# Optimization experiments

Hardware: AMD Instinct MI355X
Metric: run time of the kernel (lower is better)

The kernel has to match this reference:

```python
import jax, jax.numpy as jnp
import numpy as np

N = 50000   # nodes
E = 800000  # edges
G = 64      # graphs in batch
H = 64      # hidden_dim
IN = 4      # input_dim (degree-derived features)


def setup_inputs() -> dict:
    key = jax.random.key(0)
    ks = jax.random.split(key, 9)
    src = jax.random.randint(ks[0], (E,), 0, N, dtype=jnp.int32)
    dst = jax.random.randint(ks[1], (E,), 0, N, dtype=jnp.int32)
    graph_ids = jnp.sort(jax.random.randint(ks[2], (N,), 0, G, dtype=jnp.int32))

    def glorot(k, shape):
        fan_in = shape[0]
        return jax.random.normal(k, shape, jnp.float32) / np.float32(np.sqrt(fan_in))

    return dict(
        src=src, dst=dst, graph_ids=graph_ids,
        W1=glorot(ks[3], (IN, H)), b1=jnp.zeros((H,), jnp.float32),
        W2=glorot(ks[4], (H, H)),  b2=jnp.zeros((H,), jnp.float32),
        W3=glorot(ks[5], (H, H)),  b3=jnp.zeros((H,), jnp.float32),
        W4=glorot(ks[6], (H, H)),  b4=jnp.zeros((H,), jnp.float32),
        Wout=glorot(ks[7], (H, 1)), bout=jnp.zeros((1,), jnp.float32),
    )


def _graph_conv(h, src, dst, norm_src, norm_dst, W, b):
    # DGL GraphConv, norm='both': D_dst^{-1/2} * A^T * (D_src^{-1/2} * h) @ W + b
    m = (h * norm_src)[src]                              # [E, F] gather
    agg = jax.ops.segment_sum(m, dst, num_segments=N)    # [N, F] scatter-add
    return (agg * norm_dst) @ W + b


def reference(src, dst, graph_ids, W1, b1, W2, b2, W3, b3, W4, b4, Wout, bout):
    ones_e = jnp.ones((E,), jnp.float32)
    in_deg = jax.ops.segment_sum(ones_e, dst, num_segments=N)   # [N]
    out_deg = jax.ops.segment_sum(ones_e, src, num_segments=N)  # [N]

    # degree-derived node features (exactly as in forward)
    h1 = in_deg[:, None]
    h2 = (in_deg - 3.0 > 0).astype(jnp.float32)[:, None]
    h3 = 3.0 / h1
    h4 = (in_deg - 4.0 > 0).astype(jnp.float32)[:, None]
    h_ = jnp.concatenate([h1, h2, h3, h4], axis=1)               # [N, 4]

    # symmetric norms (DGL clamps degree to >= 1)
    norm_src = jnp.clip(out_deg, 1.0, None)[:, None] ** -0.5     # [N, 1]
    norm_dst = jnp.clip(in_deg, 1.0, None)[:, None] ** -0.5      # [N, 1]

    h = jax.nn.relu(_graph_conv(h_, src, dst, norm_src, norm_dst, W1, b1))
    h = jax.nn.relu(_graph_conv(h, src, dst, norm_src, norm_dst, W2, b2))
    h = jax.nn.relu(_graph_conv(h, src, dst, norm_src, norm_dst, W3, b3))
    h = jax.nn.relu(_graph_conv(h, src, dst, norm_src, norm_dst, W4, b4))

    # dgl.mean_nodes: per-graph mean pooling
    node_counts = jax.ops.segment_sum(jnp.ones((N,), jnp.float32), graph_ids, num_segments=G)
    graph_emb = jax.ops.segment_sum(h, graph_ids, num_segments=G) / node_counts[:, None]

    # dropout = identity at inference
    return jax.nn.sigmoid(graph_emb @ Wout + bout)               # [G, 1]
```

## Files before the change

kernel.cpp:

```cpp
#include <hip/hip_runtime.h>
#include <hip/hip_fp8.h>
#include <math.h>

#define N_NODES 50000
#define N_EDGES 800000
#define NP 4
#define NS 64
#define PSZ (N_NODES / NP)
#define SSZ (N_EDGES / NS)
#define NB 196

typedef _Float16 half8 __attribute__((ext_vector_type(8)));
typedef float floatx4 __attribute__((ext_vector_type(4)));

__device__ __forceinline__ unsigned char f_to_fp8(float f) {
    __hip_fp8_e4m3 q(f);
    return (unsigned char)q.__x;
}
__device__ __forceinline__ float fp8_to_f(unsigned char u) {
    __hip_fp8_e4m3 q;
    q.__x = (__hip_fp8_storage_t)u;
    return (float)q;
}

__global__ __launch_bounds__(256) void hist_wt_kernel(const int* __restrict__ src,
                                                      const int* __restrict__ dst,
                                                      unsigned char* __restrict__ inpart,
                                                      unsigned char* __restrict__ outpart,
                                                      unsigned char* __restrict__ rank,
                                                      const float* __restrict__ W2,
                                                      const float* __restrict__ W3,
                                                      const float* __restrict__ W4,
                                                      _Float16* __restrict__ WT,
                                                      float* __restrict__ gacc) {
    __shared__ int h[PSZ + 4];
    if (blockIdx.x >= NP * NS) {
        int wb = blockIdx.x - NP * NS;
        if (wb < 48) {
            int i = wb * 256 + threadIdx.x;
            if (i < 3 * 4096) {
                int l = i >> 12;
                int r = i & 4095;
                int k = r >> 6, n = r & 63;
                const float* W = (l == 0) ? W2 : (l == 1) ? W3 : W4;
                WT[l * 4096 + n * 64 + k] = (_Float16)W[r];
            }
        } else {
            for (int i = threadIdx.x; i < 64 * 64 + 64; i += 256) gacc[i] = 0.0f;
        }
        return;
    }
    int p = blockIdx.x / NS, s = blockIdx.x % NS;
    for (int i = threadIdx.x; i < (PSZ + 4) / 4; i += 256)
        ((int4*)h)[i] = make_int4(0, 0, 0, 0);
    __syncthreads();
    int lo = p * PSZ;
    int ebase = s * SSZ;
    const int4* d4 = (const int4*)(dst + ebase);
    const int4* s4 = (const int4*)(src + ebase);
    unsigned char* rk = rank + ebase;
    for (int i = threadIdx.x; i < SSZ / 4; i += 256) {
        int4 d = d4[i];
        int4 sv = s4[i];
        int t;
        t = d.x - lo;  if ((unsigned)t < PSZ) rk[4 * i + 0] = (unsigned char)(atomicAdd(&h[t], 1) & 0xffff);
        t = d.y - lo;  if ((unsigned)t < PSZ) rk[4 * i + 1] = (unsigned char)(atomicAdd(&h[t], 1) & 0xffff);
        t = d.z - lo;  if ((unsigned)t < PSZ) rk[4 * i + 2] = (unsigned char)(atomicAdd(&h[t], 1) & 0xffff);
        t = d.w - lo;  if ((unsigned)t < PSZ) rk[4 * i + 3] = (unsigned char)(atomicAdd(&h[t], 1) & 0xffff);
        t = sv.x - lo; if ((unsigned)t < PSZ) atomicAdd(&h[t], 0x10000);
        t = sv.y - lo; if ((unsigned)t < PSZ) atomicAdd(&h[t], 0x10000);
        t = sv.z - lo; if ((unsigned)t < PSZ) atomicAdd(&h[t], 0x10000);
        t = sv.w - lo; if ((unsigned)t < PSZ) atomicAdd(&h[t], 0x10000);
    }
    __syncthreads();
    unsigned char* ip = inpart + (size_t)s * N_NODES + lo;
    unsigned char* op = outpart + (size_t)s * N_NODES + lo;
    for (int i = threadIdx.x; i < PSZ / 2; i += 256) {
        int v0 = h[2 * i], v1 = h[2 * i + 1];
        uchar2 iv, ov;
        iv.x = (unsigned char)(v0 & 0xff);
        iv.y = (unsigned char)(v1 & 0xff);
        ov.x = (unsigned char)((v0 >> 16) & 0xff);
        ov.y = (unsigned char)((v1 >> 16) & 0xff);
        ((uchar2*)ip)[i] = iv;
        ((uchar2*)op)[i] = ov;
    }
}

__global__ void scan_block_feat_kernel(unsigned char* __restrict__ inpart,
                                       const unsigned char* __restrict__ outpart,
                                       const int* __restrict__ graph_ids,
                                       int* __restrict__ row_start, int* __restrict__ blk_sums,
                                       float* __restrict__ norm_src, float* __restrict__ norm_dst,
                                       uchar4* __restrict__ hs0, float* __restrict__ gcnt, int N) {
    __shared__ int ghist[64];
    if (threadIdx.x < 64) ghist[threadIdx.x] = 0;
    int i = blockIdx.x * 256 + threadIdx.x;
    int din_i = 0, dout_i = 0;
    if (i < N) {
        unsigned char run = 0;
#pragma unroll
        for (int s = 0; s < NS; ++s) {
            unsigned char c = inpart[(size_t)s * N_NODES + i];
            inpart[(size_t)s * N_NODES + i] = run;
            run = (unsigned char)(run + c);
            dout_i += outpart[(size_t)s * N_NODES + i];
        }
        din_i = (int)run;
        float din = (float)din_i;
        float dout = (float)dout_i;
        float ns = 1.0f / sqrtf(fmaxf(dout, 1.0f));
        float nd = 1.0f / sqrtf(fmaxf(din, 1.0f));
        norm_src[i] = ns;
        norm_dst[i] = nd;
        float h1 = din;
        float h2 = (din - 3.0f > 0.0f) ? 1.0f : 0.0f;
        float h3 = 3.0f / din;
        float h4 = (din - 4.0f > 0.0f) ? 1.0f : 0.0f;
        uchar4 q;
        q.x = f_to_fp8(h1 * ns);
        q.y = f_to_fp8(h2 * ns);
        q.z = f_to_fp8(h3 * ns);
        q.w = f_to_fp8(h4 * ns);
        hs0[i] = q;
    }
    __syncthreads();
    if (i < N) atomicAdd(&ghist[graph_ids[i]], 1);
    int lane = threadIdx.x & 63;
    int wid = threadIdx.x >> 6;
    int x = din_i;
#pragma unroll
    for (int off = 1; off < 64; off <<= 1) {
        int t = __shfl_up(x, off);
        if (lane >= off) x += t;
    }
    __shared__ int wsum[4];
    if (lane == 63) wsum[wid] = x;
    __syncthreads();
    int woff = 0;
    for (int w = 0; w < wid; ++w) woff += wsum[w];
    int incl = x + woff;
    if (i < N) row_start[i] = incl - din_i;
    if (threadIdx.x == 255) blk_sums[blockIdx.x] = incl;
    if (threadIdx.x < 64 && ghist[threadIdx.x] > 0)
        atomicAdd(&gcnt[threadIdx.x], (float)ghist[threadIdx.x]);
}

__global__ void row_add_kernel(int* __restrict__ row_start,
                               const int* __restrict__ blk_sums, int N) {
    __shared__ int sOff[256];
    int t = threadIdx.x;
    int v = (t < NB) ? blk_sums[t] : 0;
    int lane = t & 63;
    int wid = t >> 6;
    int x = v;
#pragma unroll
    for (int off = 1; off < 64; off <<= 1) {
        int tt = __shfl_up(x, off);
        if (lane >= off) x += tt;
    }
    __shared__ int wsum[4];
    if (lane == 63) wsum[wid] = x;
    __syncthreads();
    int woff = 0;
    for (int w = 0; w < wid; ++w) woff += wsum[w];
    sOff[t] = x + woff - v;
    __syncthreads();
    int i = blockIdx.x * 256 + threadIdx.x;
    if (blockIdx.x == 0 && threadIdx.x == 0) row_start[N] = N_EDGES;
    if (i < N) row_start[i] += sOff[blockIdx.x];
}

__global__ __launch_bounds__(256) void csr_fill_kernel(const int* __restrict__ src,
                                                       const int* __restrict__ dst,
                                                       const int* __restrict__ row_start,
                                                       const unsigned char* __restrict__ inpart,
                                                       const unsigned char* __restrict__ rank,
                                                       unsigned short* __restrict__ csr_src) {
    int i = blockIdx.x * 256 + threadIdx.x;
    if (i >= N_EDGES / 4) return;
    int4 d = ((const int4*)dst)[i];
    int4 sv = ((const int4*)src)[i];
    uchar4 rk = ((const uchar4*)rank)[i];
    int s = (4 * i) / SSZ;
    const unsigned char* pref = inpart + (size_t)s * N_NODES;
    csr_src[row_start[d.x] + (int)pref[d.x] + (int)rk.x] = (unsigned short)sv.x;
    csr_src[row_start[d.y] + (int)pref[d.y] + (int)rk.y] = (unsigned short)sv.y;
    csr_src[row_start[d.z] + (int)pref[d.z] + (int)rk.z] = (unsigned short)sv.z;
    csr_src[row_start[d.w] + (int)pref[d.w] + (int)rk.w] = (unsigned short)sv.w;
}

__global__ __launch_bounds__(256) void conv4_kernel(const unsigned char* __restrict__ hs0,
                                                    const int* __restrict__ row_start,
                                                    const unsigned short* __restrict__ csr_src,
                                                    const float* __restrict__ norm_src,
                                                    const float* __restrict__ norm_dst,
                                                    const float* __restrict__ W,
                                                    const float* __restrict__ b,
                                                    unsigned char* __restrict__ out, int N) {
    __shared__ float sW[4 * 64];
    __shared__ float sb[64];
    sW[threadIdx.x] = W[threadIdx.x];
    if (threadIdx.x < 64) sb[threadIdx.x] = b[threadIdx.x];

    const int lane = threadIdx.x & 63;
    const int wavei = threadIdx.x >> 6;
    const int l16 = lane & 15;
    const int node = blockIdx.x * 16 + wavei * 4 + (lane >> 4);

    const int rs = row_start[node];
    const int deg = row_start[node + 1] - rs;
    const int ncg = (deg + 15) >> 4;

    float a0 = 0.f, a1 = 0.f, a2 = 0.f, a3 = 0.f;
    for (int c = 0; c < ncg; ++c) {
        int off = c * 16 + l16;
        unsigned pos = (unsigned)(rs + off);
        if (pos > (unsigned)(N_EDGES - 1)) pos = N_EDGES - 1;
        unsigned idx = csr_src[pos];
        unsigned tv = *(const unsigned*)(hs0 + ((size_t)idx << 2));
        if (off >= deg) tv = 0u;
        a0 += fp8_to_f((unsigned char)(tv & 0xff));
        a1 += fp8_to_f((unsigned char)((tv >> 8) & 0xff));
        a2 += fp8_to_f((unsigned char)((tv >> 16) & 0xff));
        a3 += fp8_to_f((unsigned char)((tv >> 24) & 0xff));
    }
#pragma unroll
    for (int o = 1; o < 16; o <<= 1) {
        a0 += __shfl_xor(a0, o);
        a1 += __shfl_xor(a1, o);
        a2 += __shfl_xor(a2, o);
        a3 += __shfl_xor(a3, o);
    }
    __syncthreads();
    float nd = norm_dst[node];
    float ns = norm_src[node];
    uchar4 q;
    unsigned char* qp = (unsigned char*)&q;
#pragma unroll
    for (int j = 0; j < 4; ++j) {
        int f = l16 * 4 + j;
        float r = sb[f] + nd * (a0 * sW[f] + a1 * sW[64 + f] +
                                a2 * sW[128 + f] + a3 * sW[192 + f]);
        qp[j] = f_to_fp8(fmaxf(r, 0.0f) * ns);
    }
    *(uchar4*)(out + (size_t)node * 64 + l16 * 4) = q;
}

__global__ __launch_bounds__(256) void conv64_kernel(
        const unsigned char* __restrict__ hs_in,
        const int* __restrict__ row_start,
        const unsigned short* __restrict__ csr_src,
        const float* __restrict__ norm_src,
        const float* __restrict__ norm_dst,
        const _Float16* __restrict__ WT, const float* __restrict__ b,
        unsigned char* __restrict__ out8,
        const int* __restrict__ graph_ids, float* __restrict__ gacc,
        int do_pool, int N) {
    __shared__ _Float16 sAgg[16][72];
    const int lane = threadIdx.x & 63;
    const int wavei = __builtin_amdgcn_readfirstlane(threadIdx.x >> 6);
    const int l16 = lane & 15;
    const int gsel = (lane >> 4);
    const int vblock = blockIdx.x * 16;
    const int node = vblock + wavei * 4 + gsel;

    const int rs = row_start[node];
    const int deg = row_start[node + 1] - rs;

    int ncg = (deg + 15) >> 4;
    int m1 = max(ncg, __shfl_xor(ncg, 16));
    int ncw = max(m1, __shfl_xor(m1, 32));

    float acc0 = 0.f, acc1 = 0.f, acc2 = 0.f, acc3 = 0.f;
    const int blane = (lane & 48);

    int pos = rs + l16;
    unsigned pc = (unsigned)pos;
    if (pc > (unsigned)(N_EDGES - 1)) pc = N_EDGES - 1;
    int idx = (int)csr_src[pc];

    for (int c = 0; c < ncw; ++c) {
        int posN = rs + (c + 1) * 16 + l16;
        unsigned pn = (unsigned)posN;
        if (pn > (unsigned)(N_EDGES - 1)) pn = N_EDGES - 1;
        int idxN = (int)csr_src[pn];

        unsigned tv0, tv1, tv2, tv3, tv4, tv5, tv6, tv7;
        unsigned tv8, tv9, tv10, tv11, tv12, tv13, tv14, tv15;
#define GLOAD(J, TV)                                                        \
        {                                                                   \
            int si = __shfl(idx, blane + (J));                              \
            TV = *(const unsigned*)(hs_in + (((size_t)(unsigned)si) << 6)   \
                                    + (l16 << 2));                          \
        }
        GLOAD(0, tv0)   GLOAD(1, tv1)   GLOAD(2, tv2)   GLOAD(3, tv3)
        GLOAD(4, tv4)   GLOAD(5, tv5)   GLOAD(6, tv6)   GLOAD(7, tv7)
        GLOAD(8, tv8)   GLOAD(9, tv9)   GLOAD(10, tv10) GLOAD(11, tv11)
        GLOAD(12, tv12) GLOAD(13, tv13) GLOAD(14, tv14) GLOAD(15, tv15)
#undef GLOAD
        int cbase = c * 16;
#define ACC(J, TV)                                                          \
        {                                                                   \
            float mk = (cbase + (J) < deg) ? 1.0f : 0.0f;                   \
            acc0 += mk * fp8_to_f((unsigned char)(TV & 0xff));              \
            acc1 += mk * fp8_to_f((unsigned char)((TV >> 8) & 0xff));       \
            acc2 += mk * fp8_to_f((unsigned char)((TV >> 16) & 0xff));      \
            acc3 += mk * fp8_to_f((unsigned char)((TV >> 24) & 0xff));      \
        }
        ACC(0, tv0)   ACC(1, tv1)   ACC(2, tv2)   ACC(3, tv3)
        ACC(4, tv4)   ACC(5, tv5)   ACC(6, tv6)   ACC(7, tv7)
        ACC(8, tv8)   ACC(9, tv9)   ACC(10, tv10) ACC(11, tv11)
        ACC(12, tv12) ACC(13, tv13) ACC(14, tv14) ACC(15, tv15)
#undef ACC
        idx = idxN;
    }

    float nd = norm_dst[node];
    _Float16 f0 = (_Float16)(acc0 * nd);
    _Float16 f1 = (_Float16)(acc1 * nd);
    _Float16 f2 = (_Float16)(acc2 * nd);
    _Float16 f3 = (_Float16)(acc3 * nd);
    _Float16* rowp = &sAgg[wavei * 4 + gsel][l16 * 4];
    rowp[0] = f0; rowp[1] = f1; rowp[2] = f2; rowp[3] = f3;
    __syncthreads();

    const int l15 = lane & 15;
    const int quad = lane >> 4;
    const _Float16* aRow = &sAgg[l15][quad * 8];
    half8 a0 = *(const half8*)(aRow);
    half8 a1 = *(const half8*)(aRow + 32);

    const _Float16* bp = WT + ((size_t)(wavei * 16 + l15)) * 64 + quad * 8;
    half8 b0 = *(const half8*)bp;
    half8 b1 = *(const half8*)(bp + 32);

    floatx4 cc = (floatx4){0.f, 0.f, 0.f, 0.f};
    cc = __builtin_amdgcn_mfma_f32_16x16x32_f16(a0, b0, cc, 0, 0, 0);
    cc = __builtin_amdgcn_mfma_f32_16x16x32_f16(a1, b1, cc, 0, 0, 0);

    const int col = wavei * 16 + l15;
    float bias = b[col];

    if (do_pool) {
        int g0 = graph_ids[vblock];
        int g15 = graph_ids[vblock + 15];
        if (g0 == g15) {
            float fsum = 0.0f;
#pragma unroll
            for (int r = 0; r < 4; ++r)
                fsum += fmaxf(cc[r] + bias, 0.0f);
            fsum += __shfl_xor(fsum, 16);
            fsum += __shfl_xor(fsum, 32);
            if (quad == 0)
                atomicAdd(&gacc[g0 * 64 + col], fsum);
        } else {
#pragma unroll
            for (int r = 0; r < 4; ++r) {
                int m = quad * 4 + r;
                float val = fmaxf(cc[r] + bias, 0.0f);
                atomicAdd(&gacc[graph_ids[vblock + m] * 64 + col], val);
            }
        }
    } else {
#pragma unroll
        for (int r = 0; r < 4; ++r) {
            int m = quad * 4 + r;
            int v = vblock + m;
            float val = fmaxf(cc[r] + bias, 0.0f) * norm_src[v];
            out8[(size_t)v * 64 + col] = f_to_fp8(val);
        }
    }
}

__global__ void pool2_kernel(const float* __restrict__ gacc, const float* __restrict__ gcnt,
                             const float* __restrict__ Wout, const float* __restrict__ bout,
                             float* __restrict__ out) {
    int lane = threadIdx.x & 63;
    int g = blockIdx.x * 4 + (threadIdx.x >> 6);
    float p = (gacc[g * 64 + lane] / gcnt[g]) * Wout[lane];
#pragma unroll
    for (int off = 32; off; off >>= 1) p += __shfl_xor(p, off);
    if (lane == 0) out[g] = 1.0f / (1.0f + expf(-(p + bout[0])));
}

extern "C" void kernel_launch(void* const* d_in, const int* in_sizes, int n_in,
                              void* d_out, int out_size, void* d_ws, size_t ws_size,
                              hipStream_t stream) {
    const int* src = (const int*)d_in[0];
    const int* dst = (const int*)d_in[1];
    const int* graph_ids = (const int*)d_in[2];
    const float* W1 = (const float*)d_in[3];
    const float* b1 = (const float*)d_in[4];
    const float* W2 = (const float*)d_in[5];
    const float* b2 = (const float*)d_in[6];
    const float* W3 = (const float*)d_in[7];
    const float* b3 = (const float*)d_in[8];
    const float* W4 = (const float*)d_in[9];
    const float* b4 = (const float*)d_in[10];
    const float* Wout = (const float*)d_in[11];
    const float* bout = (const float*)d_in[12];
    float* out = (float*)d_out;

    const int N = N_NODES, E = N_EDGES;

    unsigned char* buf8A = (unsigned char*)d_ws;
    unsigned char* buf8B = buf8A + (size_t)N * 64;
    _Float16* WT   = (_Float16*)(buf8B + (size_t)N * 64);
    float* gacc = (float*)(WT + 3 * 4096);
    float* gcnt = gacc + 64 * 64;
    unsigned char* hs0 = (unsigned char*)(gcnt + 64);
    float* norm_src = (float*)(hs0 + (size_t)N * 4);
    float* norm_dst = norm_src + N;
    unsigned short* csr_src = (unsigned short*)(norm_dst + N);
    int* row_start = (int*)(csr_src + E);
    int* blk_sums  = row_start + (N + 1);
    unsigned char* inpart  = (unsigned char*)(blk_sums + NB + 1);
    unsigned char* outpart = inpart + (size_t)NS * N;
    unsigned char* rank    = outpart + (size_t)NS * N;

    hist_wt_kernel<<<NP * NS + 49, 256, 0, stream>>>(src, dst, inpart, outpart, rank,
                                                     W2, W3, W4, WT, gacc);
    scan_block_feat_kernel<<<NB, 256, 0, stream>>>(inpart, outpart, graph_ids,
                                                   row_start, blk_sums,
                                                   norm_src, norm_dst, (uchar4*)hs0, gcnt, N);
    row_add_kernel<<<NB, 256, 0, stream>>>(row_start, blk_sums, N);
    csr_fill_kernel<<<(E / 4 + 255) / 256, 256, 0, stream>>>(src, dst, row_start, inpart,
                                                             rank, csr_src);

    const int CB = N / 16;
    conv4_kernel<<<CB, 256, 0, stream>>>(hs0, row_start, csr_src,
                                         norm_src, norm_dst, W1, b1, buf8A, N);
    conv64_kernel<<<CB, 256, 0, stream>>>(buf8A, row_start, csr_src, norm_src, norm_dst,
                                          WT + 0 * 4096, b2, buf8B, graph_ids, gacc, 0, N);
    conv64_kernel<<<CB, 256, 0, stream>>>(buf8B, row_start, csr_src, norm_src, norm_dst,
                                          WT + 1 * 4096, b3, buf8A, graph_ids, gacc, 0, N);
    conv64_kernel<<<CB, 256, 0, stream>>>(buf8A, row_start, csr_src, norm_src, norm_dst,
                                          WT + 2 * 4096, b4, (unsigned char*)nullptr,
                                          graph_ids, gacc, 1, N);

    pool2_kernel<<<16, 256, 0, stream>>>(gacc, gcnt, Wout, bout, out);
}
```

Measured before the change: 184.3 us.

## Restructure conv64 gather to 8 lanes per node with double-buffered 8-byte loads

The 64-feature aggregation kernel now assigns 8 lanes per destination node, each loading 8 fp8 features as a uint2, so a wave covers 8 nodes instead of 4. Gathers are double-buffered: the next chunk of neighbor rows is loaded while the previous one is accumulated. Blocks shrink to 2 waves of 128 threads, and each wave does two MFMA column tiles in the dense transform. The aim is more memory-level parallelism and fewer idle lanes on low-degree nodes, at the cost of more registers per thread and more padding waste when degrees within a wave differ.

New measurement: 184.9 us. About the same (+0.4%).

```diff
diff --git a/kernel.cpp b/kernel.cpp
--- a/kernel.cpp
+++ b/kernel.cpp
@@ -247,7 +247,37 @@
     *(uchar4*)(out + (size_t)node * 64 + l16 * 4) = q;
 }
 
-__global__ __launch_bounds__(256) void conv64_kernel(
+#define GLOAD8(T, IDX)                                                     \
+    _Pragma("unroll")                                                      \
+    for (int j = 0; j < 8; ++j) {                                          \
+        int si = __shfl(IDX, blane + j);                                   \
+        T[j] = *(const uint2*)(hs_in + (((size_t)(unsigned)si) << 6)       \
+                               + (l8 << 3));                               \
+    }
+
+#define ACCUM8(T, CB)                                                      \
+    _Pragma("unroll")                                                      \
+    for (int j = 0; j < 8; ++j) {                                          \
+        float mk = ((CB) + j < deg) ? 1.0f : 0.0f;                         \
+        unsigned lo_ = T[j].x, hi_ = T[j].y;                               \
+        acc0 += mk * fp8_to_f((unsigned char)(lo_ & 0xff));                \
+        acc1 += mk * fp8_to_f((unsigned char)((lo_ >> 8) & 0xff));         \
+        acc2 += mk * fp8_to_f((unsigned char)((lo_ >> 16) & 0xff));        \
+        acc3 += mk * fp8_to_f((unsigned char)((lo_ >> 24) & 0xff));        \
+        acc4 += mk * fp8_to_f((unsigned char)(hi_ & 0xff));                \
+        acc5 += mk * fp8_to_f((unsigned char)((hi_ >> 8) & 0xff));         \
+        acc6 += mk * fp8_to_f((unsigned char)((hi_ >> 16) & 0xff));        \
+        acc7 += mk * fp8_to_f((unsigned char)((hi_ >> 24) & 0xff));        \
+    }
+
+#define LOADI8(DST, C)                                                     \
+    {                                                                      \
+        unsigned p_ = (unsigned)(rs + (C) * 8 + l8);                       \
+        if (p_ > (unsigned)(N_EDGES - 1)) p_ = N_EDGES - 1;                \
+        DST = (int)csr_src[p_];                                            \
+    }
+
+__global__ __launch_bounds__(128) void conv64_kernel(
         const unsigned char* __restrict__ hs_in,
         const int* __restrict__ row_start,
         const unsigned short* __restrict__ csr_src,
@@ -260,69 +290,51 @@
     __shared__ _Float16 sAgg[16][72];
     const int lane = threadIdx.x & 63;
     const int wavei = __builtin_amdgcn_readfirstlane(threadIdx.x >> 6);
-    const int l16 = lane & 15;
-    const int gsel = (lane >> 4);
+    const int l8 = lane & 7;
+    const int gsel = lane >> 3;
+    const int blane = lane & 56;
     const int vblock = blockIdx.x * 16;
-    const int node = vblock + wavei * 4 + gsel;
+    const int node = vblock + wavei * 8 + gsel;
 
     const int rs = row_start[node];
     const int deg = row_start[node + 1] - rs;
 
-    int ncg = (deg + 15) >> 4;
-    int m1 = max(ncg, __shfl_xor(ncg, 16));
+    int ncg = (deg + 7) >> 3;
+    int m1 = max(ncg, __shfl_xor(ncg, 8));
+    m1 = max(m1, __shfl_xor(m1, 16));
     int ncw = max(m1, __shfl_xor(m1, 32));
 
     float acc0 = 0.f, acc1 = 0.f, acc2 = 0.f, acc3 = 0.f;
-    const int blane = (lane & 48);
-
-    int pos = rs + l16;
-    unsigned pc = (unsigned)pos;
-    if (pc > (unsigned)(N_EDGES - 1)) pc = N_EDGES - 1;
-    int idx = (int)csr_src[pc];
-
-    for (int c = 0; c < ncw; ++c) {
-        int posN = rs + (c + 1) * 16 + l16;
-        unsigned pn = (unsigned)posN;
-        if (pn > (unsigned)(N_EDGES - 1)) pn = N_EDGES - 1;
-        int idxN = (int)csr_src[pn];
-
-        unsigned tv0, tv1, tv2, tv3, tv4, tv5, tv6, tv7;
-        unsigned tv8, tv9, tv10, tv11, tv12, tv13, tv14, tv15;
-#define GLOAD(J, TV)                                                        \
-        {                                                                   \
-            int si = __shfl(idx, blane + (J));                              \
-            TV = *(const unsigned*)(hs_in + (((size_t)(unsigned)si) << 6)   \
-                                    + (l16 << 2));                          \
+    float acc4 = 0.f, acc5 = 0.f, acc6 = 0.f, acc7 = 0.f;
+
+    uint2 tA[8], tB[8];
+    int idx;
+    if (ncw > 0) {
+        LOADI8(idx, 0);
+        GLOAD8(tA, idx);
+        LOADI8(idx, 1);
+        int k = 0;
+        while (k + 2 <= ncw) {
+            GLOAD8(tB, idx);
+            LOADI8(idx, k + 2);
+            ACCUM8(tA, k * 8);
+            if (k + 2 < ncw) {
+                GLOAD8(tA, idx);
+                LOADI8(idx, k + 3);
+            }
+            ACCUM8(tB, (k + 1) * 8);
+            k += 2;
         }
-        GLOAD(0, tv0)   GLOAD(1, tv1)   GLOAD(2, tv2)   GLOAD(3, tv3)
-        GLOAD(4, tv4)   GLOAD(5, tv5)   GLOAD(6, tv6)   GLOAD(7, tv7)
-        GLOAD(8, tv8)   GLOAD(9, tv9)   GLOAD(10, tv10) GLOAD(11, tv11)
-        GLOAD(12, tv12) GLOAD(13, tv13) GLOAD(14, tv14) GLOAD(15, tv15)
-#undef GLOAD
-        int cbase = c * 16;
-#define ACC(J, TV)                                                          \
-        {                                                                   \
-            float mk = (cbase + (J) < deg) ? 1.0f : 0.0f;                   \
-            acc0 += mk * fp8_to_f((unsigned char)(TV & 0xff));              \
-            acc1 += mk * fp8_to_f((unsigned char)((TV >> 8) & 0xff));       \
-            acc2 += mk * fp8_to_f((unsigned char)((TV >> 16) & 0xff));      \
-            acc3 += mk * fp8_to_f((unsigned char)((TV >> 24) & 0xff));      \
-        }
-        ACC(0, tv0)   ACC(1, tv1)   ACC(2, tv2)   ACC(3, tv3)
-        ACC(4, tv4)   ACC(5, tv5)   ACC(6, tv6)   ACC(7, tv7)
-        ACC(8, tv8)   ACC(9, tv9)   ACC(10, tv10) ACC(11, tv11)
-        ACC(12, tv12) ACC(13, tv13) ACC(14, tv14) ACC(15, tv15)
-#undef ACC
-        idx = idxN;
+        if (k < ncw) { ACCUM8(tA, k * 8); }
     }
 
     float nd = norm_dst[node];
-    _Float16 f0 = (_Float16)(acc0 * nd);
-    _Float16 f1 = (_Float16)(acc1 * nd);
-    _Float16 f2 = (_Float16)(acc2 * nd);
-    _Float16 f3 = (_Float16)(acc3 * nd);
-    _Float16* rowp = &sAgg[wavei * 4 + gsel][l16 * 4];
-    rowp[0] = f0; rowp[1] = f1; rowp[2] = f2; rowp[3] = f3;
+    half8 fv;
+    fv[0] = (_Float16)(acc0 * nd); fv[1] = (_Float16)(acc1 * nd);
+    fv[2] = (_Float16)(acc2 * nd); fv[3] = (_Float16)(acc3 * nd);
+    fv[4] = (_Float16)(acc4 * nd); fv[5] = (_Float16)(acc5 * nd);
+    fv[6] = (_Float16)(acc6 * nd); fv[7] = (_Float16)(acc7 * nd);
+    *(half8*)(&sAgg[wavei * 8 + gsel][l8 * 8]) = fv;
     __syncthreads();
 
     const int l15 = lane & 15;
@@ -331,44 +343,47 @@
     half8 a0 = *(const half8*)(aRow);
     half8 a1 = *(const half8*)(aRow + 32);
 
-    const _Float16* bp = WT + ((size_t)(wavei * 16 + l15)) * 64 + quad * 8;
-    half8 b0 = *(const half8*)bp;
-    half8 b1 = *(const half8*)(bp + 32);
-
-    floatx4 cc = (floatx4){0.f, 0.f, 0.f, 0.f};
-    cc = __builtin_amdgcn_mfma_f32_16x16x32_f16(a0, b0, cc, 0, 0, 0);
-    cc = __builtin_amdgcn_mfma_f32_16x16x32_f16(a1, b1, cc, 0, 0, 0);
-
-    const int col = wavei * 16 + l15;
-    float bias = b[col];
-
-    if (do_pool) {
-        int g0 = graph_ids[vblock];
-        int g15 = graph_ids[vblock + 15];
-        if (g0 == g15) {
-            float fsum = 0.0f;
-#pragma unroll
-            for (int r = 0; r < 4; ++r)
-                fsum += fmaxf(cc[r] + bias, 0.0f);
-            fsum += __shfl_xor(fsum, 16);
-            fsum += __shfl_xor(fsum, 32);
-            if (quad == 0)
-                atomicAdd(&gacc[g0 * 64 + col], fsum);
+#pragma unroll
+    for (int t = 0; t < 2; ++t) {
+        const int s = wavei * 2 + t;
+        const int col = s * 16 + l15;
+        const _Float16* bp = WT + ((size_t)col) * 64 + quad * 8;
+        half8 b0 = *(const half8*)bp;
+        half8 b1 = *(const half8*)(bp + 32);
+
+        floatx4 cc = (floatx4){0.f, 0.f, 0.f, 0.f};
+        cc = __builtin_amdgcn_mfma_f32_16x16x32_f16(a0, b0, cc, 0, 0, 0);
+        cc = __builtin_amdgcn_mfma_f32_16x16x32_f16(a1, b1, cc, 0, 0, 0);
+
+        float bias = b[col];
+        if (do_pool) {
+            int g0 = graph_ids[vblock];
+            int g15 = graph_ids[vblock + 15];
+            if (g0 == g15) {
+                float fsum = 0.0f;
+#pragma unroll
+                for (int r = 0; r < 4; ++r)
+                    fsum += fmaxf(cc[r] + bias, 0.0f);
+                fsum += __shfl_xor(fsum, 16);
+                fsum += __shfl_xor(fsum, 32);
+                if (quad == 0)
+                    atomicAdd(&gacc[g0 * 64 + col], fsum);
+            } else {
+#pragma unroll
+                for (int r = 0; r < 4; ++r) {
+                    int m = quad * 4 + r;
+                    float val = fmaxf(cc[r] + bias, 0.0f);
+                    atomicAdd(&gacc[graph_ids[vblock + m] * 64 + col], val);
+                }
+            }
         } else {
 #pragma unroll
             for (int r = 0; r < 4; ++r) {
                 int m = quad * 4 + r;
-                float val = fmaxf(cc[r] + bias, 0.0f);
-                atomicAdd(&gacc[graph_ids[vblock + m] * 64 + col], val);
+                int v = vblock + m;
+                float val = fmaxf(cc[r] + bias, 0.0f) * norm_src[v];
+                out8[(size_t)v * 64 + col] = f_to_fp8(val);
             }
-        }
-    } else {
-#pragma unroll
-        for (int r = 0; r < 4; ++r) {
-            int m = quad * 4 + r;
-            int v = vblock + m;
-            float val = fmaxf(cc[r] + bias, 0.0f) * norm_src[v];
-            out8[(size_t)v * 64 + col] = f_to_fp8(val);
         }
     }
 }
@@ -431,11 +446,11 @@
     const int CB = N / 16;
     conv4_kernel<<<CB, 256, 0, stream>>>(hs0, row_start, csr_src,
                                          norm_src, norm_dst, W1, b1, buf8A, N);
-    conv64_kernel<<<CB, 256, 0, stream>>>(buf8A, row_start, csr_src, norm_src, norm_dst,
+    conv64_kernel<<<CB, 128, 0, stream>>>(buf8A, row_start, csr_src, norm_src, norm_dst,
                                           WT + 0 * 4096, b2, buf8B, graph_ids, gacc, 0, N);
-    conv64_kernel<<<CB, 256, 0, stream>>>(buf8B, row_start, csr_src, norm_src, norm_dst,
+    conv64_kernel<<<CB, 128, 0, stream>>>(buf8B, row_start, csr_src, norm_src, norm_dst,
                                           WT + 1 * 4096, b3, buf8A, graph_ids, gacc, 0, N);
-    conv64_kernel<<<CB, 256, 0, stream>>>(buf8A, row_start, csr_src, norm_src, norm_dst,
+    conv64_kernel<<<CB, 128, 0, stream>>>(buf8A, row_start, csr_src, norm_src, norm_dst,
                                           WT + 2 * 4096, b4, (unsigned char*)nullptr,
                                           graph_ids, gacc, 1, N);
 
```
